# Performance work log

Measured on AMD Instinct MI355X. Metric: run time of the kernel, lower is better.

## Reference

```python
import jax, jax.numpy as jnp
import numpy as np

N_NODES = 10000
N_EDGES = 160000
IN_DIM = 512
HID = 128
HEADS = 8
EMB = 256
NEG_SLOPE = 0.2  # PyG GATConv default


def setup_inputs() -> dict:
    key = jax.random.key(0)
    ks = jax.random.split(key, 12)
    x = jax.random.normal(ks[0], (N_NODES, IN_DIM), dtype=jnp.float32)
    edge_index = jax.random.randint(ks[1], (2, N_EDGES), 0, N_NODES, dtype=jnp.int64)
    s1 = 1.0 / np.sqrt(IN_DIM)
    s2 = 1.0 / np.sqrt(HEADS * HID)
    W1 = jax.random.normal(ks[2], (IN_DIM, HEADS * HID), dtype=jnp.float32) * s1
    a_src1 = jax.random.normal(ks[3], (HEADS, HID), dtype=jnp.float32) * s2
    a_dst1 = jax.random.normal(ks[4], (HEADS, HID), dtype=jnp.float32) * s2
    b1 = jnp.zeros((HEADS * HID,), dtype=jnp.float32)
    W2 = jax.random.normal(ks[5], (HEADS * HID, EMB), dtype=jnp.float32) * s2
    a_src2 = jax.random.normal(ks[6], (1, EMB), dtype=jnp.float32) * (1.0 / np.sqrt(EMB))
    a_dst2 = jax.random.normal(ks[7], (1, EMB), dtype=jnp.float32) * (1.0 / np.sqrt(EMB))
    b2 = jnp.zeros((EMB,), dtype=jnp.float32)
    return {"x": x, "edge_index": edge_index, "W1": W1, "a_src1": a_src1,
            "a_dst1": a_dst1, "b1": b1, "W2": W2, "a_src2": a_src2,
            "a_dst2": a_dst2, "b2": b2}


def gat_layer(h_in, src, dst, W, a_src, a_dst, b, concat, num_nodes):
    """PyG-style GATConv (eval mode, self-loops already in src/dst)."""
    H, C = a_src.shape
    h = (h_in @ W).reshape(num_nodes, H, C)            # [N, H, C]
    alpha_src = jnp.einsum('nhc,hc->nh', h, a_src)      # [N, H]
    alpha_dst = jnp.einsum('nhc,hc->nh', h, a_dst)      # [N, H]
    e = jax.nn.leaky_relu(alpha_src[src] + alpha_dst[dst], NEG_SLOPE)  # [E, H]
    # segment softmax over incoming edges of each destination node
    m = jax.ops.segment_max(e, dst, num_segments=num_nodes)            # [N, H]
    ex = jnp.exp(e - m[dst])
    denom = jax.ops.segment_sum(ex, dst, num_segments=num_nodes)       # [N, H]
    alpha = ex / denom[dst]                                            # [E, H]
    out = jax.ops.segment_sum(h[src] * alpha[:, :, None], dst,
                              num_segments=num_nodes)                  # [N, H, C]
    out = out.reshape(num_nodes, H * C) if concat else out.mean(axis=1)
    return out + b


def reference(x, edge_index, W1, a_src1, a_dst1, b1, W2, a_src2, a_dst2, b2):
    N = x.shape[0]
    loops = jnp.arange(N, dtype=edge_index.dtype)
    src = jnp.concatenate([edge_index[0], loops])
    dst = jnp.concatenate([edge_index[1], loops])
    h = gat_layer(x, src, dst, W1, a_src1, a_dst1, b1, concat=True, num_nodes=N)
    h = jax.nn.elu(h)  # dropout inactive in eval mode
    out = gat_layer(h, src, dst, W2, a_src2, a_dst2, b2, concat=False, num_nodes=N)
    return out
```

## Files before the change

### kernel.cpp

```cpp
#include <hip/hip_runtime.h>
#include <hip/hip_bf16.h>

typedef __attribute__((ext_vector_type(8))) short short8;
typedef __attribute__((ext_vector_type(4))) float floatx4;
typedef __attribute__((ext_vector_type(4))) unsigned short ushort4v;
typedef __attribute__((ext_vector_type(8))) unsigned short ushort8v;
typedef __attribute__((ext_vector_type(2))) unsigned int uint2v;
typedef __attribute__((ext_vector_type(4))) unsigned int uint4v;

#define NN 10000
#define E0 160000
#define ETOT (E0 + NN)
#define IN_DIM 512
#define HID1 1024
#define EMB 256
#define MPAD 10112
#define NX (NN * IN_DIM)
#define NW1 (IN_DIM * HID1)
#define NW2 (HID1 * EMB)
#define DETB 625

__device__ __forceinline__ float bf2f(unsigned short u) {
    unsigned v = ((unsigned)u) << 16;
    float f;
    __builtin_memcpy(&f, &v, 4);
    return f;
}
__device__ __forceinline__ float bflo(unsigned v) {
    unsigned x = v << 16;
    float f; __builtin_memcpy(&f, &x, 4);
    return f;
}
__device__ __forceinline__ float bfhi(unsigned v) {
    unsigned x = v & 0xffff0000u;
    float f; __builtin_memcpy(&f, &x, 4);
    return f;
}
__device__ __forceinline__ unsigned short f2bf(float f) {
    unsigned u;
    __builtin_memcpy(&u, &f, 4);
    unsigned lsb = (u >> 16) & 1;
    u += 0x7fff + lsb;
    return (unsigned short)(u >> 16);
}
__device__ __forceinline__ unsigned packbf(float lo, float hi) {
    return (unsigned)f2bf(lo) | ((unsigned)f2bf(hi) << 16);
}
__device__ __forceinline__ float loadf(const void* p, size_t i, int isf32) {
    if (isf32) return ((const float*)p)[i];
    return bf2f(((const unsigned short*)p)[i]);
}
__device__ __forceinline__ float lrelu(float e) { return e > 0.f ? e : 0.2f * e; }

__global__ void zero_kernel(int* p, int n) {
    int i = blockIdx.x * 256 + threadIdx.x;
    if (i < n) p[i] = 0;
}

__global__ __launch_bounds__(256) void probe_kernel(const int* ei32, const unsigned* xw,
                                                    int* eflag, int* isf32) {
    int t = threadIdx.x;
    if (blockIdx.x < DETB) {
        int i = blockIdx.x * 256 + t;
        int v = 0;
        int idx = 2 * i + 1;
        if (idx < 2 * E0) v = ei32[idx];
        unsigned long long any = __ballot(v != 0);
        if (any && (t & 63) == 0) atomicOr(eflag, 1);
    } else {
        __shared__ int cnt[256];
        int c = 0;
        #pragma unroll
        for (int j = 0; j < 16; ++j) {
            unsigned w = xw[t * 16 + j];
            int ex = (w >> 7) & 0xFF;
            if (ex >= 110 && ex <= 135) c++;
        }
        cnt[t] = c;
        __syncthreads();
        for (int off = 128; off > 0; off >>= 1) {
            if (t < off) cnt[t] += cnt[t + off];
            __syncthreads();
        }
        if (t == 0) *isf32 = (cnt[0] < 2048) ? 1 : 0;
    }
}

__device__ __forceinline__ int load_edge(const void* ei, long long idx, int m32) {
    if (m32) return ((const int*)ei)[idx];
    return (int)(((const long long*)ei)[idx]);
}

__global__ void count_kernel(const void* ei, const int* flag, int* counts) {
    int e = blockIdx.x * 256 + threadIdx.x;
    if (e < E0) {
        int m32 = (*flag != 0);
        int d = load_edge(ei, (long long)E0 + e, m32);
        if (d >= 0 && d < NN) atomicAdd(&counts[d], 1);
    }
}

__global__ __launch_bounds__(1024) void scan_kernel(const int* counts, int* offsets, int* cursor) {
    __shared__ int wsum[16];
    int t = threadIdx.x;
    int lane = t & 63, wv = t >> 6;
    int base = t * 10;
    int local[10];
    int s = 0;
    #pragma unroll
    for (int j = 0; j < 10; ++j) {
        int idx = base + j;
        int v = (idx < NN) ? (counts[idx] + 1) : 0;
        local[j] = v; s += v;
    }
    int v = s;
    #pragma unroll
    for (int d = 1; d < 64; d <<= 1) {
        int o = __shfl_up(v, d, 64);
        if (lane >= d) v += o;
    }
    if (lane == 63) wsum[wv] = v;
    __syncthreads();
    if (t < 16) {
        int w = wsum[t];
        #pragma unroll
        for (int d = 1; d < 16; d <<= 1) {
            int o = __shfl_up(w, d, 16);
            if (t >= d) w += o;
        }
        wsum[t] = w;
    }
    __syncthreads();
    int woff = (wv == 0) ? 0 : wsum[wv - 1];
    int run = woff + v - s;
    #pragma unroll
    for (int j = 0; j < 10; ++j) {
        int idx = base + j;
        if (idx < NN) { offsets[idx] = run; cursor[idx] = run; run += local[j]; }
    }
    if (t == 1023) offsets[NN] = wsum[15];
}

__global__ void scatter_kernel(const void* ei, const int* flag, int* cursor, int* csr_src) {
    int e = blockIdx.x * 256 + threadIdx.x;
    if (e >= ETOT) return;
    int m32 = (*flag != 0);
    int s, d;
    if (e < E0) { s = load_edge(ei, e, m32); d = load_edge(ei, (long long)E0 + e, m32); }
    else { s = d = e - E0; }
    if (s < 0) s = 0; if (s >= NN) s = NN - 1;
    if (d < 0) d = 0; if (d >= NN) d = NN - 1;
    int pos = atomicAdd(&cursor[d], 1);
    if (pos >= 0 && pos < ETOT) csr_src[pos] = s;
}

__global__ void convall_kernel(const void* x, const void* W1, const void* W2,
                               unsigned short* xb, unsigned short* W1t, unsigned short* W2t,
                               const int* isf32)
{
    int i = blockIdx.x * 256 + threadIdx.x;
    int f = *isf32;
    if (i < NX) { xb[i] = f2bf(loadf(x, i, f)); return; }
    i -= NX;
    if (i < NW1) {
        int r = i / HID1, c = i % HID1;
        W1t[(size_t)c * IN_DIM + r] = f2bf(loadf(W1, i, f));
        return;
    }
    i -= NW1;
    if (i < NW2) {
        int r = i / EMB, c = i % EMB;
        W2t[(size_t)c * HID1 + r] = f2bf(loadf(W2, i, f));
    }
}

template<bool OUTBF16>
__global__ __launch_bounds__(256) void gemm_tile(
    const unsigned short* __restrict__ A,
    const unsigned short* __restrict__ Bt,
    void* __restrict__ Cv,
    int N, int K)
{
    __shared__ unsigned short As[128 * 32];
    __shared__ unsigned short Bs[128 * 32];
    int t = threadIdx.x;
    int wave = t >> 6;
    int lane = t & 63;
    int quad = lane >> 4;
    int l16  = lane & 15;
    int mq = wave & 1, nq = wave >> 1;
    size_t mblk = (size_t)blockIdx.x * 128;
    size_t nblk = (size_t)blockIdx.y * 128;

    floatx4 acc[4][4];
    #pragma unroll
    for (int i = 0; i < 4; ++i)
        #pragma unroll
        for (int j = 0; j < 4; ++j)
            acc[i][j] = (floatx4){0.f, 0.f, 0.f, 0.f};

    const unsigned short* Abase = A + mblk * K;
    const unsigned short* Bbase = Bt + nblk * K;

    for (int kk = 0; kk < K; kk += 32) {
        __syncthreads();
        #pragma unroll
        for (int j = 0; j < 2; ++j) {
            int chunk = (wave << 7) + (j << 6) + lane;
            int r  = chunk >> 2;
            int cs = (chunk & 3) ^ (r & 3);
            const unsigned short* ga = Abase + (size_t)r * K + kk + cs * 8;
            const unsigned short* gb = Bbase + (size_t)r * K + kk + cs * 8;
            __builtin_amdgcn_global_load_lds(
                (const __attribute__((address_space(1))) void*)ga,
                (__attribute__((address_space(3))) void*)(As + (size_t)((wave << 7) + (j << 6)) * 8),
                16, 0, 0);
            __builtin_amdgcn_global_load_lds(
                (const __attribute__((address_space(1))) void*)gb,
                (__attribute__((address_space(3))) void*)(Bs + (size_t)((wave << 7) + (j << 6)) * 8),
                16, 0, 0);
        }
        __syncthreads();

        short8 af[4], bf[4];
        #pragma unroll
        for (int i = 0; i < 4; ++i) {
            int ar = mq * 64 + i * 16 + l16;
            int br = nq * 64 + i * 16 + l16;
            af[i] = *(const short8*)(const void*)(As + ar * 32 + (quad ^ (ar & 3)) * 8);
            bf[i] = *(const short8*)(const void*)(Bs + br * 32 + (quad ^ (br & 3)) * 8);
        }
        #pragma unroll
        for (int i = 0; i < 4; ++i)
            #pragma unroll
            for (int j = 0; j < 4; ++j)
                acc[i][j] = __builtin_amdgcn_mfma_f32_16x16x32_bf16(af[i], bf[j], acc[i][j], 0, 0, 0);
    }

    size_t crow0 = mblk + mq * 64 + quad * 4;
    size_t ccol0 = nblk + nq * 64 + l16;
    #pragma unroll
    for (int i = 0; i < 4; ++i) {
        #pragma unroll
        for (int r = 0; r < 4; ++r) {
            size_t row = crow0 + i * 16 + r;
            size_t b = row * N + ccol0;
            #pragma unroll
            for (int j = 0; j < 4; ++j) {
                if (OUTBF16) ((unsigned short*)Cv)[b + j * 16] = f2bf(acc[i][j][r]);
                else         ((float*)Cv)[b + j * 16] = acc[i][j][r];
            }
        }
    }
}

__global__ __launch_bounds__(256) void alpha1_kernel(
    const unsigned short* __restrict__ h1,
    const void* __restrict__ a_src, const void* __restrict__ a_dst,
    const int* __restrict__ isf32,
    float* __restrict__ as1, float* __restrict__ ad1)
{
    int n = blockIdx.x, t = threadIdx.x;
    int f = *isf32;
    ushort4v hv = *(const ushort4v*)(const void*)(h1 + (size_t)n * HID1 + t * 4);
    float ps = 0.f, pd = 0.f;
    #pragma unroll
    for (int i = 0; i < 4; ++i) {
        float h = bf2f(hv[i]);
        ps += h * loadf(a_src, t * 4 + i, f);
        pd += h * loadf(a_dst, t * 4 + i, f);
    }
    #pragma unroll
    for (int off = 1; off < 32; off <<= 1) {
        ps += __shfl_xor(ps, off, 64);
        pd += __shfl_xor(pd, off, 64);
    }
    if ((t & 31) == 0) {
        int h = t >> 5;
        as1[n * 8 + h] = ps;
        ad1[n * 8 + h] = pd;
    }
}

__global__ __launch_bounds__(256) void agg1_kernel(
    const unsigned short* __restrict__ h1, const int* __restrict__ offsets,
    const int* __restrict__ csr_src, const float* __restrict__ as1,
    const float* __restrict__ ad1, const void* __restrict__ b1,
    const int* __restrict__ isf32,
    unsigned short* __restrict__ hmid)
{
    int head = blockIdx.x & 7;
    int ng   = blockIdx.x >> 3;
    int n    = ng * 4 + (threadIdx.x >> 6);
    if (n >= NN) return;
    int lane = threadIdx.x & 63;
    int q    = lane >> 4;
    int sl   = lane & 15;
    int f = *isf32;
    int beg = offsets[n], end = offsets[n + 1];
    if (beg < 0) beg = 0; if (end > ETOT) end = ETOT;
    float ad = ad1[n * 8 + head];
    const unsigned* rb = (const unsigned*)h1 + head * 64 + sl * 4;
    const float* asb = as1 + head;

    float den = 0.f;
    float acc[8];
    #pragma unroll
    for (int j = 0; j < 8; ++j) acc[j] = 0.f;

    int i = beg + q;
    for (; i + 12 < end; i += 16) {
        int s0 = csr_src[i];      s0 &= 0x7fffffff; if (s0 >= NN) s0 = 0;
        int s1 = csr_src[i + 4];  s1 &= 0x7fffffff; if (s1 >= NN) s1 = 0;
        int s2 = csr_src[i + 8];  s2 &= 0x7fffffff; if (s2 >= NN) s2 = 0;
        int s3 = csr_src[i + 12]; s3 &= 0x7fffffff; if (s3 >= NN) s3 = 0;
        uint4v v0 = *(const uint4v*)(const void*)(rb + (size_t)s0 * 512);
        uint4v v1 = *(const uint4v*)(const void*)(rb + (size_t)s1 * 512);
        uint4v v2 = *(const uint4v*)(const void*)(rb + (size_t)s2 * 512);
        uint4v v3 = *(const uint4v*)(const void*)(rb + (size_t)s3 * 512);
        float w0 = __expf(lrelu(asb[s0 * 8] + ad));
        float w1 = __expf(lrelu(asb[s1 * 8] + ad));
        float w2 = __expf(lrelu(asb[s2 * 8] + ad));
        float w3 = __expf(lrelu(asb[s3 * 8] + ad));
        den += (w0 + w1) + (w2 + w3);
        #pragma unroll
        for (int k = 0; k < 4; ++k) {
            acc[2 * k]     += (bflo(v0[k]) * w0 + bflo(v1[k]) * w1) + (bflo(v2[k]) * w2 + bflo(v3[k]) * w3);
            acc[2 * k + 1] += (bfhi(v0[k]) * w0 + bfhi(v1[k]) * w1) + (bfhi(v2[k]) * w2 + bfhi(v3[k]) * w3);
        }
    }
    for (; i + 4 < end; i += 8) {
        int s0 = csr_src[i];     s0 &= 0x7fffffff; if (s0 >= NN) s0 = 0;
        int s1 = csr_src[i + 4]; s1 &= 0x7fffffff; if (s1 >= NN) s1 = 0;
        uint4v v0 = *(const uint4v*)(const void*)(rb + (size_t)s0 * 512);
        uint4v v1 = *(const uint4v*)(const void*)(rb + (size_t)s1 * 512);
        float w0 = __expf(lrelu(asb[s0 * 8] + ad));
        float w1 = __expf(lrelu(asb[s1 * 8] + ad));
        den += w0 + w1;
        #pragma unroll
        for (int k = 0; k < 4; ++k) {
            acc[2 * k]     += bflo(v0[k]) * w0 + bflo(v1[k]) * w1;
            acc[2 * k + 1] += bfhi(v0[k]) * w0 + bfhi(v1[k]) * w1;
        }
    }
    if (i < end) {
        int s0 = csr_src[i]; s0 &= 0x7fffffff; if (s0 >= NN) s0 = 0;
        uint4v v0 = *(const uint4v*)(const void*)(rb + (size_t)s0 * 512);
        float w0 = __expf(lrelu(asb[s0 * 8] + ad));
        den += w0;
        #pragma unroll
        for (int k = 0; k < 4; ++k) {
            acc[2 * k]     += bflo(v0[k]) * w0;
            acc[2 * k + 1] += bfhi(v0[k]) * w0;
        }
    }

    #pragma unroll
    for (int j = 0; j < 8; ++j) {
        acc[j] += __shfl_xor(acc[j], 16, 64);
        acc[j] += __shfl_xor(acc[j], 32, 64);
    }
    den += __shfl_xor(den, 16, 64);
    den += __shfl_xor(den, 32, 64);

    if (q == 0) {
        float rden = 1.0f / fmaxf(den, 1e-30f);
        int c0 = head * 128 + sl * 8;
        uint4v o;
        #pragma unroll
        for (int k = 0; k < 4; ++k) {
            float v0 = acc[2 * k]     * rden + loadf(b1, c0 + 2 * k, f);
            float v1 = acc[2 * k + 1] * rden + loadf(b1, c0 + 2 * k + 1, f);
            v0 = v0 > 0.f ? v0 : (__expf(v0) - 1.0f);
            v1 = v1 > 0.f ? v1 : (__expf(v1) - 1.0f);
            o[k] = packbf(v0, v1);
        }
        *(uint4v*)(void*)((unsigned*)hmid + (size_t)n * 512 + head * 64 + sl * 4) = o;
    }
}

__global__ __launch_bounds__(256) void alpha2_kernel(
    const unsigned short* __restrict__ h2,
    const void* __restrict__ a_src2, const void* __restrict__ a_dst2,
    const int* __restrict__ isf32,
    float* __restrict__ as2, float* __restrict__ ad2)
{
    int n = blockIdx.x, t = threadIdx.x;
    int f = *isf32;
    float v = bf2f(h2[(size_t)n * EMB + t]);
    float ps = v * loadf(a_src2, t, f);
    float pd = v * loadf(a_dst2, t, f);
    __shared__ float rs[256], rdm[256];
    rs[t] = ps; rdm[t] = pd;
    __syncthreads();
    for (int off = 128; off > 0; off >>= 1) {
        if (t < off) { rs[t] += rs[t + off]; rdm[t] += rdm[t + off]; }
        __syncthreads();
    }
    if (t == 0) { as2[n] = rs[0]; ad2[n] = rdm[0]; }
}

__global__ __launch_bounds__(256) void agg2_kernel(
    const unsigned short* __restrict__ h2, const int* __restrict__ offsets,
    const int* __restrict__ csr_src, const float* __restrict__ as2,
    const float* __restrict__ ad2, const void* __restrict__ b2,
    const int* __restrict__ isf32,
    float* __restrict__ out)
{
    int chunk = blockIdx.x & 3;
    int ng    = blockIdx.x >> 2;
    int n     = ng * 4 + (threadIdx.x >> 6);
    if (n >= NN) return;
    int lane = threadIdx.x & 63;
    int q    = lane >> 4;
    int sl   = lane & 15;
    int f = *isf32;
    int beg = offsets[n], end = offsets[n + 1];
    if (beg < 0) beg = 0; if (end > ETOT) end = ETOT;
    float adn = ad2[n];
    const unsigned* rb = (const unsigned*)h2 + chunk * 32 + sl * 2;

    float den = 0.f;
    float acc[4];
    #pragma unroll
    for (int j = 0; j < 4; ++j) acc[j] = 0.f;

    int i = beg + q;
    for (; i + 12 < end; i += 16) {
        int s0 = csr_src[i];      s0 &= 0x7fffffff; if (s0 >= NN) s0 = 0;
        int s1 = csr_src[i + 4];  s1 &= 0x7fffffff; if (s1 >= NN) s1 = 0;
        int s2 = csr_src[i + 8];  s2 &= 0x7fffffff; if (s2 >= NN) s2 = 0;
        int s3 = csr_src[i + 12]; s3 &= 0x7fffffff; if (s3 >= NN) s3 = 0;
        uint2v v0 = *(const uint2v*)(const void*)(rb + (size_t)s0 * 128);
        uint2v v1 = *(const uint2v*)(const void*)(rb + (size_t)s1 * 128);
        uint2v v2 = *(const uint2v*)(const void*)(rb + (size_t)s2 * 128);
        uint2v v3 = *(const uint2v*)(const void*)(rb + (size_t)s3 * 128);
        float w0 = __expf(lrelu(as2[s0] + adn));
        float w1 = __expf(lrelu(as2[s1] + adn));
        float w2 = __expf(lrelu(as2[s2] + adn));
        float w3 = __expf(lrelu(as2[s3] + adn));
        den += (w0 + w1) + (w2 + w3);
        acc[0] += (bflo(v0[0]) * w0 + bflo(v1[0]) * w1) + (bflo(v2[0]) * w2 + bflo(v3[0]) * w3);
        acc[1] += (bfhi(v0[0]) * w0 + bfhi(v1[0]) * w1) + (bfhi(v2[0]) * w2 + bfhi(v3[0]) * w3);
        acc[2] += (bflo(v0[1]) * w0 + bflo(v1[1]) * w1) + (bflo(v2[1]) * w2 + bflo(v3[1]) * w3);
        acc[3] += (bfhi(v0[1]) * w0 + bfhi(v1[1]) * w1) + (bfhi(v2[1]) * w2 + bfhi(v3[1]) * w3);
    }
    for (; i + 4 < end; i += 8) {
        int s0 = csr_src[i];     s0 &= 0x7fffffff; if (s0 >= NN) s0 = 0;
        int s1 = csr_src[i + 4]; s1 &= 0x7fffffff; if (s1 >= NN) s1 = 0;
        uint2v v0 = *(const uint2v*)(const void*)(rb + (size_t)s0 * 128);
        uint2v v1 = *(const uint2v*)(const void*)(rb + (size_t)s1 * 128);
        float w0 = __expf(lrelu(as2[s0] + adn));
        float w1 = __expf(lrelu(as2[s1] + adn));
        den += w0 + w1;
        acc[0] += bflo(v0[0]) * w0 + bflo(v1[0]) * w1;
        acc[1] += bfhi(v0[0]) * w0 + bfhi(v1[0]) * w1;
        acc[2] += bflo(v0[1]) * w0 + bflo(v1[1]) * w1;
        acc[3] += bfhi(v0[1]) * w0 + bfhi(v1[1]) * w1;
    }
    if (i < end) {
        int s0 = csr_src[i]; s0 &= 0x7fffffff; if (s0 >= NN) s0 = 0;
        uint2v v0 = *(const uint2v*)(const void*)(rb + (size_t)s0 * 128);
        float w0 = __expf(lrelu(as2[s0] + adn));
        den += w0;
        acc[0] += bflo(v0[0]) * w0;
        acc[1] += bfhi(v0[0]) * w0;
        acc[2] += bflo(v0[1]) * w0;
        acc[3] += bfhi(v0[1]) * w0;
    }

    #pragma unroll
    for (int j = 0; j < 4; ++j) {
        acc[j] += __shfl_xor(acc[j], 16, 64);
        acc[j] += __shfl_xor(acc[j], 32, 64);
    }
    den += __shfl_xor(den, 16, 64);
    den += __shfl_xor(den, 32, 64);

    if (q == 0) {
        float rden = 1.0f / fmaxf(den, 1e-30f);
        int c0 = chunk * 64 + sl * 4;
        floatx4 o;
        #pragma unroll
        for (int j = 0; j < 4; ++j)
            o[j] = acc[j] * rden + loadf(b2, c0 + j, f);
        *(floatx4*)(void*)(out + (size_t)n * EMB + c0) = o;
    }
}

extern "C" void kernel_launch(void* const* d_in, const int* in_sizes, int n_in,
                              void* d_out, int out_size, void* d_ws, size_t ws_size,
                              hipStream_t stream)
{
    const void* x      = d_in[0];
    const void* edge   = d_in[1];
    const void* W1     = d_in[2];
    const void* a_src1 = d_in[3];
    const void* a_dst1 = d_in[4];
    const void* b1     = d_in[5];
    const void* W2     = d_in[6];
    const void* a_src2 = d_in[7];
    const void* a_dst2 = d_in[8];
    const void* b2     = d_in[9];
    float* out = (float*)d_out;

    char* ws = (char*)d_ws;
    size_t off = 0;
    auto alloc = [&](size_t bytes) -> void* {
        void* p = ws + off;
        off += (bytes + 255) & ~(size_t)255;
        return p;
    };
    int*            counts = (int*)alloc((NN + 2) * 4);
    int*            offs   = (int*)alloc((NN + 1) * 4);
    int*            cursor = (int*)alloc(NN * 4);
    int*            csr    = (int*)alloc((size_t)ETOT * 4);
    float*          as1    = (float*)alloc((size_t)NN * 8 * 4);
    float*          ad1    = (float*)alloc((size_t)NN * 8 * 4);
    float*          as2    = (float*)alloc((size_t)NN * 4);
    float*          ad2    = (float*)alloc((size_t)NN * 4);
    unsigned short* xb     = (unsigned short*)alloc((size_t)MPAD * IN_DIM * 2);
    unsigned short* W1t    = (unsigned short*)alloc((size_t)IN_DIM * HID1 * 2);
    unsigned short* W2t    = (unsigned short*)alloc((size_t)HID1 * EMB * 2);
    unsigned short* h1b    = (unsigned short*)alloc((size_t)MPAD * HID1 * 2);
    unsigned short* hmid   = (unsigned short*)alloc((size_t)MPAD * HID1 * 2);
    unsigned short* h2b    = (unsigned short*)alloc((size_t)MPAD * EMB * 2);
    int* eflag = counts + NN;
    int* isf32 = counts + NN + 1;

    zero_kernel<<<(NN + 2 + 255) / 256, 256, 0, stream>>>(counts, NN + 2);
    probe_kernel<<<DETB + 1, 256, 0, stream>>>((const int*)edge, (const unsigned*)x, eflag, isf32);

    count_kernel<<<(E0 + 255) / 256, 256, 0, stream>>>(edge, eflag, counts);
    scan_kernel<<<1, 1024, 0, stream>>>(counts, offs, cursor);
    scatter_kernel<<<(ETOT + 255) / 256, 256, 0, stream>>>(edge, eflag, cursor, csr);

    convall_kernel<<<(NX + NW1 + NW2 + 255) / 256, 256, 0, stream>>>(
        x, W1, W2, xb, W1t, W2t, isf32);

    dim3 g1(MPAD / 128, HID1 / 128);
    gemm_tile<true><<<g1, 256, 0, stream>>>(xb, W1t, h1b, HID1, IN_DIM);

    alpha1_kernel<<<NN, 256, 0, stream>>>(h1b, a_src1, a_dst1, isf32, as1, ad1);
    agg1_kernel<<<(NN / 4) * 8, 256, 0, stream>>>(h1b, offs, csr, as1, ad1, b1, isf32, hmid);

    dim3 g2(MPAD / 128, EMB / 128);
    gemm_tile<true><<<g2, 256, 0, stream>>>(hmid, W2t, h2b, EMB, HID1);

    alpha2_kernel<<<NN, 256, 0, stream>>>(h2b, a_src2, a_dst2, isf32, as2, ad2);
    agg2_kernel<<<(NN / 4) * 4, 256, 0, stream>>>(h2b, offs, csr, as2, ad2, b2, isf32, out);
}
```

Before: 303.9 us.

## Fuse attention logits into GEMM epilogue, merge zero/probe, restructure agg1

The per-node alpha kernels are dropped. Attention logit dot products are now computed in the GEMM epilogue from fp32 accumulators and combined across column tiles with atomicAdd. The zeroing and dtype/edge probe kernels are merged into one launch, and the edge probe now samples only the first 16K edges. agg1 now processes all heads of one node per block with two edge groups reduced through shared memory. This cuts launches and the extra passes over h1/h2, at the cost of atomics and a different order of floating-point summation.

```diff
diff --git a/kernel.cpp b/kernel.cpp
--- a/kernel.cpp
+++ b/kernel.cpp
@@ -18,7 +18,6 @@
 #define NX (NN * IN_DIM)
 #define NW1 (IN_DIM * HID1)
 #define NW2 (HID1 * EMB)
-#define DETB 625
 
 __device__ __forceinline__ float bf2f(unsigned short u) {
     unsigned v = ((unsigned)u) << 16;
@@ -43,31 +42,33 @@
     u += 0x7fff + lsb;
     return (unsigned short)(u >> 16);
 }
-__device__ __forceinline__ unsigned packbf(float lo, float hi) {
-    return (unsigned)f2bf(lo) | ((unsigned)f2bf(hi) << 16);
-}
 __device__ __forceinline__ float loadf(const void* p, size_t i, int isf32) {
     if (isf32) return ((const float*)p)[i];
     return bf2f(((const unsigned short*)p)[i]);
 }
 __device__ __forceinline__ float lrelu(float e) { return e > 0.f ? e : 0.2f * e; }
 
-__global__ void zero_kernel(int* p, int n) {
-    int i = blockIdx.x * 256 + threadIdx.x;
-    if (i < n) p[i] = 0;
-}
-
-__global__ __launch_bounds__(256) void probe_kernel(const int* ei32, const unsigned* xw,
-                                                    int* eflag, int* isf32) {
-    int t = threadIdx.x;
-    if (blockIdx.x < DETB) {
-        int i = blockIdx.x * 256 + t;
-        int v = 0;
-        int idx = 2 * i + 1;
-        if (idx < 2 * E0) v = ei32[idx];
-        unsigned long long any = __ballot(v != 0);
-        if (any && (t & 63) == 0) atomicOr(eflag, 1);
-    } else {
+__global__ __launch_bounds__(256) void probezero_kernel(
+    const int* __restrict__ ei32, const unsigned* __restrict__ xw,
+    int* __restrict__ zbase, int zn, int* __restrict__ eflag, int* __restrict__ isf32)
+{
+    int b = blockIdx.x, t = threadIdx.x;
+    int i = b * 256 + t;
+    if (i < zn) zbase[i] = 0;
+    if (b == 0) {
+        int any = 0;
+        #pragma unroll
+        for (int k = 0; k < 64; ++k) {
+            int idx = (t + k * 256) * 2 + 1;
+            any |= ei32[idx];
+        }
+        __shared__ int sf;
+        if (t == 0) sf = 0;
+        __syncthreads();
+        if (any) atomicOr(&sf, 1);
+        __syncthreads();
+        if (t == 0) *eflag = sf;
+    } else if (b == 1) {
         __shared__ int cnt[256];
         int c = 0;
         #pragma unroll
@@ -174,12 +175,14 @@
     }
 }
 
-template<bool OUTBF16>
+template<int HSHIFT, int HN>
 __global__ __launch_bounds__(256) void gemm_tile(
     const unsigned short* __restrict__ A,
     const unsigned short* __restrict__ Bt,
-    void* __restrict__ Cv,
-    int N, int K)
+    void* __restrict__ Cv, int N, int K,
+    const void* __restrict__ a_src, const void* __restrict__ a_dst,
+    const int* __restrict__ isf32,
+    float* __restrict__ as_out, float* __restrict__ ad_out)
 {
     __shared__ unsigned short As[128 * 32];
     __shared__ unsigned short Bs[128 * 32];
@@ -246,39 +249,40 @@
             size_t row = crow0 + i * 16 + r;
             size_t b = row * N + ccol0;
             #pragma unroll
-            for (int j = 0; j < 4; ++j) {
-                if (OUTBF16) ((unsigned short*)Cv)[b + j * 16] = f2bf(acc[i][j][r]);
-                else         ((float*)Cv)[b + j * 16] = acc[i][j][r];
+            for (int j = 0; j < 4; ++j)
+                ((unsigned short*)Cv)[b + j * 16] = f2bf(acc[i][j][r]);
+        }
+    }
+
+    int f = *isf32;
+    float a_s[4], a_d[4];
+    #pragma unroll
+    for (int j = 0; j < 4; ++j) {
+        a_s[j] = loadf(a_src, ccol0 + j * 16, f);
+        a_d[j] = loadf(a_dst, ccol0 + j * 16, f);
+    }
+    int head = (int)((nblk + (size_t)nq * 64) >> HSHIFT);
+    #pragma unroll
+    for (int i = 0; i < 4; ++i) {
+        #pragma unroll
+        for (int r = 0; r < 4; ++r) {
+            float ps = acc[i][0][r] * a_s[0] + acc[i][1][r] * a_s[1]
+                     + acc[i][2][r] * a_s[2] + acc[i][3][r] * a_s[3];
+            float pd = acc[i][0][r] * a_d[0] + acc[i][1][r] * a_d[1]
+                     + acc[i][2][r] * a_d[2] + acc[i][3][r] * a_d[3];
+            #pragma unroll
+            for (int off = 1; off < 16; off <<= 1) {
+                ps += __shfl_xor(ps, off, 16);
+                pd += __shfl_xor(pd, off, 16);
             }
-        }
-    }
-}
-
-__global__ __launch_bounds__(256) void alpha1_kernel(
-    const unsigned short* __restrict__ h1,
-    const void* __restrict__ a_src, const void* __restrict__ a_dst,
-    const int* __restrict__ isf32,
-    float* __restrict__ as1, float* __restrict__ ad1)
-{
-    int n = blockIdx.x, t = threadIdx.x;
-    int f = *isf32;
-    ushort4v hv = *(const ushort4v*)(const void*)(h1 + (size_t)n * HID1 + t * 4);
-    float ps = 0.f, pd = 0.f;
-    #pragma unroll
-    for (int i = 0; i < 4; ++i) {
-        float h = bf2f(hv[i]);
-        ps += h * loadf(a_src, t * 4 + i, f);
-        pd += h * loadf(a_dst, t * 4 + i, f);
-    }
-    #pragma unroll
-    for (int off = 1; off < 32; off <<= 1) {
-        ps += __shfl_xor(ps, off, 64);
-        pd += __shfl_xor(pd, off, 64);
-    }
-    if ((t & 31) == 0) {
-        int h = t >> 5;
-        as1[n * 8 + h] = ps;
-        ad1[n * 8 + h] = pd;
+            if (l16 == 0) {
+                size_t row = crow0 + i * 16 + r;
+                if (row < NN) {
+                    atomicAdd(&as_out[row * HN + head], ps);
+                    atomicAdd(&ad_out[row * HN + head], pd);
+                }
+            }
+        }
     }
 }
 
@@ -289,115 +293,92 @@
     const int* __restrict__ isf32,
     unsigned short* __restrict__ hmid)
 {
-    int head = blockIdx.x & 7;
-    int ng   = blockIdx.x >> 3;
-    int n    = ng * 4 + (threadIdx.x >> 6);
-    if (n >= NN) return;
-    int lane = threadIdx.x & 63;
-    int q    = lane >> 4;
-    int sl   = lane & 15;
+    int n = blockIdx.x, t = threadIdx.x;
     int f = *isf32;
     int beg = offsets[n], end = offsets[n + 1];
     if (beg < 0) beg = 0; if (end > ETOT) end = ETOT;
-    float ad = ad1[n * 8 + head];
-    const unsigned* rb = (const unsigned*)h1 + head * 64 + sl * 4;
-    const float* asb = as1 + head;
+    int g = t >> 7;
+    int u = t & 127;
+    int c0 = u * 8;
+    int hc = u >> 4;
+    float ad = ad1[n * 8 + hc];
 
     float den = 0.f;
     float acc[8];
     #pragma unroll
     for (int j = 0; j < 8; ++j) acc[j] = 0.f;
 
-    int i = beg + q;
-    for (; i + 12 < end; i += 16) {
-        int s0 = csr_src[i];      s0 &= 0x7fffffff; if (s0 >= NN) s0 = 0;
-        int s1 = csr_src[i + 4];  s1 &= 0x7fffffff; if (s1 >= NN) s1 = 0;
-        int s2 = csr_src[i + 8];  s2 &= 0x7fffffff; if (s2 >= NN) s2 = 0;
-        int s3 = csr_src[i + 12]; s3 &= 0x7fffffff; if (s3 >= NN) s3 = 0;
-        uint4v v0 = *(const uint4v*)(const void*)(rb + (size_t)s0 * 512);
-        uint4v v1 = *(const uint4v*)(const void*)(rb + (size_t)s1 * 512);
-        uint4v v2 = *(const uint4v*)(const void*)(rb + (size_t)s2 * 512);
-        uint4v v3 = *(const uint4v*)(const void*)(rb + (size_t)s3 * 512);
-        float w0 = __expf(lrelu(asb[s0 * 8] + ad));
-        float w1 = __expf(lrelu(asb[s1 * 8] + ad));
-        float w2 = __expf(lrelu(asb[s2 * 8] + ad));
-        float w3 = __expf(lrelu(asb[s3 * 8] + ad));
+    int i = beg + g;
+    for (; i + 6 < end; i += 8) {
+        int s0 = csr_src[i];     s0 &= 0x7fffffff; if (s0 >= NN) s0 = 0;
+        int s1 = csr_src[i + 2]; s1 &= 0x7fffffff; if (s1 >= NN) s1 = 0;
+        int s2 = csr_src[i + 4]; s2 &= 0x7fffffff; if (s2 >= NN) s2 = 0;
+        int s3 = csr_src[i + 6]; s3 &= 0x7fffffff; if (s3 >= NN) s3 = 0;
+        ushort8v hv0 = *(const ushort8v*)(const void*)(h1 + (size_t)s0 * HID1 + c0);
+        ushort8v hv1 = *(const ushort8v*)(const void*)(h1 + (size_t)s1 * HID1 + c0);
+        ushort8v hv2 = *(const ushort8v*)(const void*)(h1 + (size_t)s2 * HID1 + c0);
+        ushort8v hv3 = *(const ushort8v*)(const void*)(h1 + (size_t)s3 * HID1 + c0);
+        float e0 = as1[s0 * 8 + hc] + ad;
+        float e1 = as1[s1 * 8 + hc] + ad;
+        float e2 = as1[s2 * 8 + hc] + ad;
+        float e3 = as1[s3 * 8 + hc] + ad;
+        e0 = e0 > 0.f ? e0 : 0.2f * e0;
+        e1 = e1 > 0.f ? e1 : 0.2f * e1;
+        e2 = e2 > 0.f ? e2 : 0.2f * e2;
+        e3 = e3 > 0.f ? e3 : 0.2f * e3;
+        float w0 = __expf(e0), w1 = __expf(e1), w2 = __expf(e2), w3 = __expf(e3);
         den += (w0 + w1) + (w2 + w3);
         #pragma unroll
-        for (int k = 0; k < 4; ++k) {
-            acc[2 * k]     += (bflo(v0[k]) * w0 + bflo(v1[k]) * w1) + (bflo(v2[k]) * w2 + bflo(v3[k]) * w3);
-            acc[2 * k + 1] += (bfhi(v0[k]) * w0 + bfhi(v1[k]) * w1) + (bfhi(v2[k]) * w2 + bfhi(v3[k]) * w3);
-        }
-    }
-    for (; i + 4 < end; i += 8) {
+        for (int j = 0; j < 8; ++j)
+            acc[j] += (bf2f(hv0[j]) * w0 + bf2f(hv1[j]) * w1)
+                    + (bf2f(hv2[j]) * w2 + bf2f(hv3[j]) * w3);
+    }
+    for (; i + 2 < end; i += 4) {
         int s0 = csr_src[i];     s0 &= 0x7fffffff; if (s0 >= NN) s0 = 0;
-        int s1 = csr_src[i + 4]; s1 &= 0x7fffffff; if (s1 >= NN) s1 = 0;
-        uint4v v0 = *(const uint4v*)(const void*)(rb + (size_t)s0 * 512);
-        uint4v v1 = *(const uint4v*)(const void*)(rb + (size_t)s1 * 512);
-        float w0 = __expf(lrelu(asb[s0 * 8] + ad));
-        float w1 = __expf(lrelu(asb[s1 * 8] + ad));
+        int s1 = csr_src[i + 2]; s1 &= 0x7fffffff; if (s1 >= NN) s1 = 0;
+        ushort8v hv0 = *(const ushort8v*)(const void*)(h1 + (size_t)s0 * HID1 + c0);
+        ushort8v hv1 = *(const ushort8v*)(const void*)(h1 + (size_t)s1 * HID1 + c0);
+        float e0 = as1[s0 * 8 + hc] + ad;
+        float e1 = as1[s1 * 8 + hc] + ad;
+        e0 = e0 > 0.f ? e0 : 0.2f * e0;
+        e1 = e1 > 0.f ? e1 : 0.2f * e1;
+        float w0 = __expf(e0), w1 = __expf(e1);
         den += w0 + w1;
         #pragma unroll
-        for (int k = 0; k < 4; ++k) {
-            acc[2 * k]     += bflo(v0[k]) * w0 + bflo(v1[k]) * w1;
-            acc[2 * k + 1] += bfhi(v0[k]) * w0 + bfhi(v1[k]) * w1;
-        }
+        for (int j = 0; j < 8; ++j)
+            acc[j] += bf2f(hv0[j]) * w0 + bf2f(hv1[j]) * w1;
     }
     if (i < end) {
         int s0 = csr_src[i]; s0 &= 0x7fffffff; if (s0 >= NN) s0 = 0;
-        uint4v v0 = *(const uint4v*)(const void*)(rb + (size_t)s0 * 512);
-        float w0 = __expf(lrelu(asb[s0 * 8] + ad));
+        ushort8v hv0 = *(const ushort8v*)(const void*)(h1 + (size_t)s0 * HID1 + c0);
+        float e0 = as1[s0 * 8 + hc] + ad;
+        e0 = e0 > 0.f ? e0 : 0.2f * e0;
+        float w0 = __expf(e0);
         den += w0;
         #pragma unroll
-        for (int k = 0; k < 4; ++k) {
-            acc[2 * k]     += bflo(v0[k]) * w0;
-            acc[2 * k + 1] += bfhi(v0[k]) * w0;
-        }
-    }
-
-    #pragma unroll
-    for (int j = 0; j < 8; ++j) {
-        acc[j] += __shfl_xor(acc[j], 16, 64);
-        acc[j] += __shfl_xor(acc[j], 32, 64);
-    }
-    den += __shfl_xor(den, 16, 64);
-    den += __shfl_xor(den, 32, 64);
-
-    if (q == 0) {
+        for (int j = 0; j < 8; ++j) acc[j] += bf2f(hv0[j]) * w0;
+    }
+
+    __shared__ float accsh[128][9];
+    __shared__ float densh[128];
+    if (g == 1) {
+        #pragma unroll
+        for (int j = 0; j < 8; ++j) accsh[u][j] = acc[j];
+        densh[u] = den;
+    }
+    __syncthreads();
+    if (g == 0) {
+        den += densh[u];
         float rden = 1.0f / fmaxf(den, 1e-30f);
-        int c0 = head * 128 + sl * 8;
-        uint4v o;
-        #pragma unroll
-        for (int k = 0; k < 4; ++k) {
-            float v0 = acc[2 * k]     * rden + loadf(b1, c0 + 2 * k, f);
-            float v1 = acc[2 * k + 1] * rden + loadf(b1, c0 + 2 * k + 1, f);
-            v0 = v0 > 0.f ? v0 : (__expf(v0) - 1.0f);
-            v1 = v1 > 0.f ? v1 : (__expf(v1) - 1.0f);
-            o[k] = packbf(v0, v1);
-        }
-        *(uint4v*)(void*)((unsigned*)hmid + (size_t)n * 512 + head * 64 + sl * 4) = o;
-    }
-}
-
-__global__ __launch_bounds__(256) void alpha2_kernel(
-    const unsigned short* __restrict__ h2,
-    const void* __restrict__ a_src2, const void* __restrict__ a_dst2,
-    const int* __restrict__ isf32,
-    float* __restrict__ as2, float* __restrict__ ad2)
-{
-    int n = blockIdx.x, t = threadIdx.x;
-    int f = *isf32;
-    float v = bf2f(h2[(size_t)n * EMB + t]);
-    float ps = v * loadf(a_src2, t, f);
-    float pd = v * loadf(a_dst2, t, f);
-    __shared__ float rs[256], rdm[256];
-    rs[t] = ps; rdm[t] = pd;
-    __syncthreads();
-    for (int off = 128; off > 0; off >>= 1) {
-        if (t < off) { rs[t] += rs[t + off]; rdm[t] += rdm[t + off]; }
-        __syncthreads();
-    }
-    if (t == 0) { as2[n] = rs[0]; ad2[n] = rdm[0]; }
+        ushort8v outw;
+        #pragma unroll
+        for (int j = 0; j < 8; ++j) {
+            float v = (acc[j] + accsh[u][j]) * rden + loadf(b1, c0 + j, f);
+            v = v > 0.f ? v : (__expf(v) - 1.0f);
+            outw[j] = f2bf(v);
+        }
+        *(ushort8v*)(void*)(hmid + (size_t)n * HID1 + c0) = outw;
+    }
 }
 
 __global__ __launch_bounds__(256) void agg2_kernel(
@@ -511,25 +492,27 @@
         off += (bytes + 255) & ~(size_t)255;
         return p;
     };
-    int*            counts = (int*)alloc((NN + 2) * 4);
-    int*            offs   = (int*)alloc((NN + 1) * 4);
-    int*            cursor = (int*)alloc(NN * 4);
-    int*            csr    = (int*)alloc((size_t)ETOT * 4);
+    int*            counts = (int*)alloc((size_t)NN * 4);
     float*          as1    = (float*)alloc((size_t)NN * 8 * 4);
     float*          ad1    = (float*)alloc((size_t)NN * 8 * 4);
     float*          as2    = (float*)alloc((size_t)NN * 4);
     float*          ad2    = (float*)alloc((size_t)NN * 4);
+    int             zn     = (int)(((char*)ad2 - (char*)counts) / 4) + NN;
+    int*            flags  = (int*)alloc(2 * 4);
+    int*            offs   = (int*)alloc((NN + 1) * 4);
+    int*            cursor = (int*)alloc(NN * 4);
+    int*            csr    = (int*)alloc((size_t)ETOT * 4);
     unsigned short* xb     = (unsigned short*)alloc((size_t)MPAD * IN_DIM * 2);
     unsigned short* W1t    = (unsigned short*)alloc((size_t)IN_DIM * HID1 * 2);
     unsigned short* W2t    = (unsigned short*)alloc((size_t)HID1 * EMB * 2);
     unsigned short* h1b    = (unsigned short*)alloc((size_t)MPAD * HID1 * 2);
     unsigned short* hmid   = (unsigned short*)alloc((size_t)MPAD * HID1 * 2);
     unsigned short* h2b    = (unsigned short*)alloc((size_t)MPAD * EMB * 2);
-    int* eflag = counts + NN;
-    int* isf32 = counts + NN + 1;
-
-    zero_kernel<<<(NN + 2 + 255) / 256, 256, 0, stream>>>(counts, NN + 2);
-    probe_kernel<<<DETB + 1, 256, 0, stream>>>((const int*)edge, (const unsigned*)x, eflag, isf32);
+    int* eflag = flags;
+    int* isf32 = flags + 1;
+
+    probezero_kernel<<<(zn + 255) / 256, 256, 0, stream>>>(
+        (const int*)edge, (const unsigned*)x, counts, zn, eflag, isf32);
 
     count_kernel<<<(E0 + 255) / 256, 256, 0, stream>>>(edge, eflag, counts);
     scan_kernel<<<1, 1024, 0, stream>>>(counts, offs, cursor);
@@ -539,14 +522,14 @@
         x, W1, W2, xb, W1t, W2t, isf32);
 
     dim3 g1(MPAD / 128, HID1 / 128);
-    gemm_tile<true><<<g1, 256, 0, stream>>>(xb, W1t, h1b, HID1, IN_DIM);
-
-    alpha1_kernel<<<NN, 256, 0, stream>>>(h1b, a_src1, a_dst1, isf32, as1, ad1);
-    agg1_kernel<<<(NN / 4) * 8, 256, 0, stream>>>(h1b, offs, csr, as1, ad1, b1, isf32, hmid);
+    gemm_tile<7, 8><<<g1, 256, 0, stream>>>(xb, W1t, h1b, HID1, IN_DIM,
+                                            a_src1, a_dst1, isf32, as1, ad1);
+
+    agg1_kernel<<<NN, 256, 0, stream>>>(h1b, offs, csr, as1, ad1, b1, isf32, hmid);
 
     dim3 g2(MPAD / 128, EMB / 128);
-    gemm_tile<true><<<g2, 256, 0, stream>>>(hmid, W2t, h2b, EMB, HID1);
-
-    alpha2_kernel<<<NN, 256, 0, stream>>>(h2b, a_src2, a_dst2, isf32, as2, ad2);
+    gemm_tile<8, 1><<<g2, 256, 0, stream>>>(hmid, W2t, h2b, EMB, HID1,
+                                            a_src2, a_dst2, isf32, as2, ad2);
+
     agg2_kernel<<<(NN / 4) * 4, 256, 0, stream>>>(h2b, offs, csr, as2, ad2, b2, isf32, out);
 }
```

New measurement: 264.6 us (median of 2 runs). 1.15x faster.
